# Kernel tuning notes

Hardware: AMD Instinct MI355X
Metric: run time of the kernel (lower is better)

## Reference

```python
import jax, jax.numpy as jnp
import numpy as np

K = 16          # top-k edges kept per node (init kwarg k)
TEMP = 1.0      # gumbel-softmax temperature
NEG = -1e9


def setup_inputs() -> dict:
    key = jax.random.key(0)
    ks = jax.random.split(key, 12)
    N, E, D, ED, H1, H2, OUT = 4096, 131072, 8, 8, 16, 16, 112
    x = jax.random.normal(ks[0], (N, D), jnp.float32)
    edge_index = jax.random.randint(ks[1], (2, E), 0, N, dtype=jnp.int64)
    edge_attr = jax.random.normal(ks[2], (E, ED), jnp.float32)
    node_mask = jnp.ones((N,), jnp.int32)
    # learned params
    mlp_w = jax.random.normal(ks[3], (1, ED + 2 * D), jnp.float32) * 0.1
    mlp_b = jnp.zeros((1,), jnp.float32)
    w1 = jax.random.normal(ks[4], (D, H1), jnp.float32) * (1.0 / np.sqrt(D))
    b1 = jnp.zeros((H1,), jnp.float32)
    w2 = jax.random.normal(ks[5], (H1, H2), jnp.float32) * (1.0 / np.sqrt(H1))
    b2 = jnp.zeros((H2,), jnp.float32)
    fc_w = jax.random.normal(ks[6], (H2, OUT), jnp.float32) * (1.0 / np.sqrt(H2))
    fc_b = jnp.zeros((OUT,), jnp.float32)
    return {"num_nodes": N, "edge_index": edge_index, "edge_attr": edge_attr,
            "x": x, "node_mask": node_mask, "mlp_w": mlp_w, "mlp_b": mlp_b,
            "w1": w1, "b1": b1, "w2": w2, "b2": b2, "fc_w": fc_w, "fc_b": fc_b}


def reference(num_nodes, edge_index, edge_attr, x, node_mask,
              mlp_w, mlp_b, w1, b1, w2, b2, fc_w, fc_b):
    N = num_nodes
    D = x.shape[1]
    row, col = edge_index[0], edge_index[1]

    # dense adjacency indicator (original: sparse_coo -> to_dense; used only via adj != 0)
    adj = jnp.zeros((N, N), x.dtype).at[row, col].set(1.0)

    # Linear MLP over concat([node_emb, neighbor_emb, edge_emb]) decomposes:
    # score[u,v] = x_u.w_node + adj[u,v]*(x_v.w_nbr) + (e_uv.w_edge) + b
    w_node = mlp_w[0, :D]
    w_nbr = mlp_w[0, D:2 * D]
    w_edge = mlp_w[0, 2 * D:]
    edge_s = jnp.zeros((N, N), x.dtype).at[row, col].set(edge_attr @ w_edge)
    score = (x @ w_node)[:, None] + adj * (x @ w_nbr)[None, :] + edge_s + mlp_b[0]

    score = jnp.where(adj > 0, score, NEG)
    z = jax.nn.softmax(score, axis=-1)
    z = jnp.where(adj > 0, z, NEG)
    # eval mode: gumbel noise = 0
    z = jax.nn.softmax(z / TEMP, axis=-1)

    vals, idx = jax.lax.top_k(z, K)          # (N, K)
    kth = vals[:, -1]
    topk_mask = jnp.zeros((N, N), bool).at[jnp.arange(N)[:, None], idx].set(True)

    # per-edge keep mask -> expressed as edge weight 0/1 (static shapes)
    keep = (node_mask[row] != 0) & (kth[row] != 0) & topk_mask[row, col]
    w_e = keep.astype(x.dtype)

    def gcn_conv(h, W, b):
        hW = h @ W
        deg = jnp.zeros((N,), h.dtype).at[col].add(w_e) + 1.0   # +1 self loop
        dinv = jax.lax.rsqrt(deg)
        coef = w_e * dinv[row] * dinv[col]
        agg = jnp.zeros((N, hW.shape[1]), h.dtype).at[col].add(coef[:, None] * hW[row])
        return agg + (dinv * dinv)[:, None] * hW + b            # self-loop term + bias

    # GCN (eval mode => dropout is identity)
    h = jax.nn.relu(gcn_conv(x, w1, b1))
    h = gcn_conv(h, w2, b2)
    h = jax.nn.relu(h)
    out = h @ fc_w + fc_b
    # node_mask is all ones, so x[node_mask != 0] == x
    return out
```

## Files before the change

### kernel.cpp

```cpp
#include <hip/hip_runtime.h>
#include <stdint.h>

#define N_NODES 4096
#define N_EDGES 131072
#define D_IN    8
#define NH      16
#define N_OUT   112
#define TOPK    16
#define CAP_ROW 128
#define CAP_COL 64

__global__ __launch_bounds__(256) void k_pre(
        const int* __restrict__ ei, const float* __restrict__ ea,
        const float* __restrict__ x, const float* __restrict__ mlp_w,
        const float* __restrict__ w1,
        float* __restrict__ s_nbr, float* __restrict__ h1W,
        int* __restrict__ deg_row, unsigned* __restrict__ csr,
        float* __restrict__ csr_ew) {
    int b = blockIdx.x;
    if (b < N_EDGES / 256) {
        int e = b * 256 + threadIdx.x;
        float s = 0.f;
#pragma unroll
        for (int d = 0; d < D_IN; ++d) s += ea[e * D_IN + d] * mlp_w[2 * D_IN + d];
        int r = ei[e];
        int c = ei[N_EDGES + e];
        int slot = atomicAdd(&deg_row[r], 1);
        if (slot < CAP_ROW) {
            csr[r * CAP_ROW + slot] = ((unsigned)e << 12) | (unsigned)c;
            csr_ew[r * CAP_ROW + slot] = s;
        }
    } else {
        int i = (b - N_EDGES / 256) * 256 + threadIdx.x;
        if (i >= N_NODES) return;
        float xv[D_IN];
#pragma unroll
        for (int d = 0; d < D_IN; ++d) xv[d] = x[i * D_IN + d];
        float s = 0.f;
#pragma unroll
        for (int d = 0; d < D_IN; ++d) s += xv[d] * mlp_w[D_IN + d];
        s_nbr[i] = s;
#pragma unroll
        for (int j = 0; j < NH; ++j) {
            float a = 0.f;
#pragma unroll
            for (int d = 0; d < D_IN; ++d) a += xv[d] * w1[d * NH + j];
            h1W[i * NH + j] = a;
        }
    }
}

__global__ __launch_bounds__(64) void k_topk(
        const unsigned* __restrict__ csr, const float* __restrict__ csr_ew,
        const int* __restrict__ deg_row, const float* __restrict__ s_nbr,
        const int* __restrict__ node_mask,
        int* __restrict__ deg_in, int* __restrict__ csc) {
    __shared__ unsigned s_pk[CAP_ROW];
    __shared__ float s_v[CAP_ROW];
    __shared__ unsigned char s_rep[CAP_ROW];
    __shared__ unsigned char s_kept[CAP_ROW];
    __shared__ int s_distinct;
    int r = blockIdx.x;
    int t = threadIdx.x;
    int n = deg_row[r];
    if (n > CAP_ROW) n = CAP_ROW;
    if (n == 0) return;
    for (int k = t; k < n; k += 64) {
        unsigned pk = csr[r * CAP_ROW + k];
        s_pk[k] = pk;
        s_v[k] = s_nbr[pk & 4095u] + csr_ew[r * CAP_ROW + k];
    }
    __syncthreads();
    for (int k = t; k < n; k += 64) {
        unsigned pk = s_pk[k], c = pk & 4095u;
        unsigned char rep = 1;
        for (int j = 0; j < n; ++j) {
            unsigned pj = s_pk[j];
            if ((pj & 4095u) == c && pj > pk) { rep = 0; break; }
        }
        s_rep[k] = rep;
    }
    __syncthreads();
    if (t == 0) {
        int c = 0;
        for (int j = 0; j < n; ++j) c += s_rep[j];
        s_distinct = c;
    }
    __syncthreads();
    if (s_distinct < TOPK || node_mask[r] == 0) return;
    for (int k = t; k < n; k += 64) {
        unsigned char kept = 0;
        if (s_rep[k]) {
            float vk = s_v[k];
            unsigned ck = s_pk[k] & 4095u;
            int beats = 0;
            for (int j = 0; j < n; ++j) {
                if (!s_rep[j]) continue;
                float vj = s_v[j];
                unsigned cj = s_pk[j] & 4095u;
                if (vj > vk || (vj == vk && cj < ck)) ++beats;
            }
            kept = (beats < TOPK);
        }
        s_kept[k] = kept;
    }
    __syncthreads();
    for (int k = t; k < n; k += 64) {
        unsigned c = s_pk[k] & 4095u;
        unsigned char kp = 0;
        for (int j = 0; j < n; ++j) {
            if ((s_pk[j] & 4095u) == c && s_rep[j]) { kp = s_kept[j]; break; }
        }
        if (kp) {
            int p = atomicAdd(&deg_in[(int)c], 1);
            if (p < CAP_COL) csc[(int)c * CAP_COL + p] = r;
        }
    }
}

__global__ __launch_bounds__(256) void k_gather1(
        const int* __restrict__ csc, const int* __restrict__ deg_in,
        const float* __restrict__ h1W, const float* __restrict__ b1,
        const float* __restrict__ w2, float* __restrict__ h2W) {
    int idx = blockIdx.x * 256 + threadIdx.x;
    int c = idx >> 4, f = idx & 15;
    int m = deg_in[c];
    int mm = m > CAP_COL ? CAP_COL : m;
    float acc = 0.f;
    for (int j = 0; j < mm; ++j) {
        int r = csc[c * CAP_COL + j];
        acc += rsqrtf(1.0f + (float)deg_in[r]) * h1W[r * NH + f];
    }
    float dc = rsqrtf(1.0f + (float)m);
    float v = dc * acc + dc * dc * h1W[c * NH + f] + b1[f];
    float h = v > 0.f ? v : 0.f;
    int lane = threadIdx.x & 63;
    int base = lane & 48;
    float a = 0.f;
#pragma unroll
    for (int ff = 0; ff < NH; ++ff) {
        float hv = __shfl(h, base | ff, 64);
        a += hv * w2[ff * NH + f];
    }
    h2W[c * NH + f] = a;
}

__global__ __launch_bounds__(128) void k_out(
        const int* __restrict__ csc, const int* __restrict__ deg_in,
        const float* __restrict__ h2W, const float* __restrict__ b2,
        const float* __restrict__ fc_w, const float* __restrict__ fc_b,
        float* __restrict__ out) {
    __shared__ float sh[NH];
    int c = blockIdx.x;
    int t = threadIdx.x;
    if (t < NH) {
        int m = deg_in[c];
        int mm = m > CAP_COL ? CAP_COL : m;
        float acc = 0.f;
        for (int j = 0; j < mm; ++j) {
            int r = csc[c * CAP_COL + j];
            acc += rsqrtf(1.0f + (float)deg_in[r]) * h2W[r * NH + t];
        }
        float dc = rsqrtf(1.0f + (float)m);
        float v = dc * acc + dc * dc * h2W[c * NH + t] + b2[t];
        sh[t] = v > 0.f ? v : 0.f;
    }
    __syncthreads();
    if (t < N_OUT) {
        float a = fc_b[t];
#pragma unroll
        for (int ff = 0; ff < NH; ++ff) a += sh[ff] * fc_w[ff * N_OUT + t];
        out[c * N_OUT + t] = a;
    }
}

extern "C" void kernel_launch(void* const* d_in, const int* in_sizes, int n_in,
                              void* d_out, int out_size, void* d_ws, size_t ws_size,
                              hipStream_t stream) {
    const int*   ei        = (const int*)d_in[1];
    const float* ea        = (const float*)d_in[2];
    const float* x         = (const float*)d_in[3];
    const int*   node_mask = (const int*)d_in[4];
    const float* mlp_w     = (const float*)d_in[5];
    const float* w1        = (const float*)d_in[7];
    const float* b1        = (const float*)d_in[8];
    const float* w2        = (const float*)d_in[9];
    const float* b2        = (const float*)d_in[10];
    const float* fcw       = (const float*)d_in[11];
    const float* fcb       = (const float*)d_in[12];
    float* out = (float*)d_out;

    char* ws = (char*)d_ws;
    size_t off = 0;
    auto alloc = [&](size_t bytes) -> void* {
        void* p = ws + off;
        off += (bytes + 511) & ~(size_t)511;
        return p;
    };
    int*      deg_row = (int*)alloc(N_NODES * 4);
    int*      deg_in  = (int*)alloc(N_NODES * 4);
    size_t zero_bytes = off;
    float*    s_nbr  = (float*)alloc(N_NODES * 4);
    float*    h1W    = (float*)alloc(N_NODES * NH * 4);
    float*    h2W    = (float*)alloc(N_NODES * NH * 4);
    unsigned* csr    = (unsigned*)alloc(N_NODES * CAP_ROW * 4);
    float*    csr_ew = (float*)alloc(N_NODES * CAP_ROW * 4);
    int*      csc    = (int*)alloc(N_NODES * CAP_COL * 4);
    (void)ws_size; (void)in_sizes; (void)n_in; (void)out_size;

    hipMemsetAsync(d_ws, 0, zero_bytes, stream);

    k_pre<<<N_EDGES / 256 + N_NODES / 256, 256, 0, stream>>>(
        ei, ea, x, mlp_w, w1, s_nbr, h1W, deg_row, csr, csr_ew);
    k_topk<<<N_NODES, 64, 0, stream>>>(
        csr, csr_ew, deg_row, s_nbr, node_mask, deg_in, csc);
    k_gather1<<<(N_NODES * NH) / 256, 256, 0, stream>>>(
        csc, deg_in, h1W, b1, w2, h2W);
    k_out<<<N_NODES, 128, 0, stream>>>(
        csc, deg_in, h2W, b2, fcw, fcb, out);
}
```

Measured before the change: 143.9 us.

## Fuse all stages into one cooperative persistent kernel with grid syncs

Replaces the memset and four separate kernel launches with a single cooperative kernel of 512 blocks of 256 threads. Grid-wide syncs separate zeroing, edge/CSR build, top-k selection, the first GCN layer and the output layer. This removes launch and memset overhead. In exchange it adds grid barrier costs and less parallelism per phase, since top-k now runs 4 rows per block per iteration with block-wide syncs. The output stage is also remapped to 16 threads per node.

New measurement: 383.5 us. +166.5%, slower.

```diff
diff --git a/kernel.cpp b/kernel.cpp
--- a/kernel.cpp
+++ b/kernel.cpp
@@ -1,5 +1,8 @@
 #include <hip/hip_runtime.h>
+#include <hip/hip_cooperative_groups.h>
 #include <stdint.h>
+
+namespace cg = cooperative_groups;
 
 #define N_NODES 4096
 #define N_EDGES 131072
@@ -10,16 +13,28 @@
 #define CAP_ROW 128
 #define CAP_COL 64
 
-__global__ __launch_bounds__(256) void k_pre(
+#define NBLK 512
+#define NTHR 256
+
+__global__ __launch_bounds__(256) void k_fused(
         const int* __restrict__ ei, const float* __restrict__ ea,
-        const float* __restrict__ x, const float* __restrict__ mlp_w,
-        const float* __restrict__ w1,
+        const float* __restrict__ x, const int* __restrict__ node_mask,
+        const float* __restrict__ mlp_w, const float* __restrict__ w1,
+        const float* __restrict__ b1, const float* __restrict__ w2,
+        const float* __restrict__ b2, const float* __restrict__ fc_w,
+        const float* __restrict__ fc_b, float* __restrict__ out,
+        int* __restrict__ deg_row, int* __restrict__ deg_in,
         float* __restrict__ s_nbr, float* __restrict__ h1W,
-        int* __restrict__ deg_row, unsigned* __restrict__ csr,
-        float* __restrict__ csr_ew) {
-    int b = blockIdx.x;
-    if (b < N_EDGES / 256) {
-        int e = b * 256 + threadIdx.x;
+        float* __restrict__ h2W, unsigned* __restrict__ csr,
+        float* __restrict__ csr_ew, int* __restrict__ csc) {
+    cg::grid_group grid = cg::this_grid();
+    const int tid = blockIdx.x * NTHR + threadIdx.x;
+
+    if (tid < N_NODES) { deg_row[tid] = 0; deg_in[tid] = 0; }
+    grid.sync();
+
+    {
+        const int e = tid;
         float s = 0.f;
 #pragma unroll
         for (int d = 0; d < D_IN; ++d) s += ea[e * D_IN + d] * mlp_w[2 * D_IN + d];
@@ -30,147 +45,147 @@
             csr[r * CAP_ROW + slot] = ((unsigned)e << 12) | (unsigned)c;
             csr_ew[r * CAP_ROW + slot] = s;
         }
-    } else {
-        int i = (b - N_EDGES / 256) * 256 + threadIdx.x;
-        if (i >= N_NODES) return;
+    }
+    if (tid < N_NODES) {
         float xv[D_IN];
 #pragma unroll
-        for (int d = 0; d < D_IN; ++d) xv[d] = x[i * D_IN + d];
+        for (int d = 0; d < D_IN; ++d) xv[d] = x[tid * D_IN + d];
         float s = 0.f;
 #pragma unroll
         for (int d = 0; d < D_IN; ++d) s += xv[d] * mlp_w[D_IN + d];
-        s_nbr[i] = s;
+        s_nbr[tid] = s;
 #pragma unroll
         for (int j = 0; j < NH; ++j) {
             float a = 0.f;
 #pragma unroll
             for (int d = 0; d < D_IN; ++d) a += xv[d] * w1[d * NH + j];
-            h1W[i * NH + j] = a;
-        }
-    }
-}
-
-__global__ __launch_bounds__(64) void k_topk(
-        const unsigned* __restrict__ csr, const float* __restrict__ csr_ew,
-        const int* __restrict__ deg_row, const float* __restrict__ s_nbr,
-        const int* __restrict__ node_mask,
-        int* __restrict__ deg_in, int* __restrict__ csc) {
-    __shared__ unsigned s_pk[CAP_ROW];
-    __shared__ float s_v[CAP_ROW];
-    __shared__ unsigned char s_rep[CAP_ROW];
-    __shared__ unsigned char s_kept[CAP_ROW];
-    __shared__ int s_distinct;
-    int r = blockIdx.x;
-    int t = threadIdx.x;
-    int n = deg_row[r];
-    if (n > CAP_ROW) n = CAP_ROW;
-    if (n == 0) return;
-    for (int k = t; k < n; k += 64) {
-        unsigned pk = csr[r * CAP_ROW + k];
-        s_pk[k] = pk;
-        s_v[k] = s_nbr[pk & 4095u] + csr_ew[r * CAP_ROW + k];
-    }
-    __syncthreads();
-    for (int k = t; k < n; k += 64) {
-        unsigned pk = s_pk[k], c = pk & 4095u;
-        unsigned char rep = 1;
-        for (int j = 0; j < n; ++j) {
-            unsigned pj = s_pk[j];
-            if ((pj & 4095u) == c && pj > pk) { rep = 0; break; }
-        }
-        s_rep[k] = rep;
-    }
-    __syncthreads();
-    if (t == 0) {
-        int c = 0;
-        for (int j = 0; j < n; ++j) c += s_rep[j];
-        s_distinct = c;
-    }
-    __syncthreads();
-    if (s_distinct < TOPK || node_mask[r] == 0) return;
-    for (int k = t; k < n; k += 64) {
-        unsigned char kept = 0;
-        if (s_rep[k]) {
-            float vk = s_v[k];
-            unsigned ck = s_pk[k] & 4095u;
-            int beats = 0;
-            for (int j = 0; j < n; ++j) {
-                if (!s_rep[j]) continue;
-                float vj = s_v[j];
-                unsigned cj = s_pk[j] & 4095u;
-                if (vj > vk || (vj == vk && cj < ck)) ++beats;
-            }
-            kept = (beats < TOPK);
-        }
-        s_kept[k] = kept;
-    }
-    __syncthreads();
-    for (int k = t; k < n; k += 64) {
-        unsigned c = s_pk[k] & 4095u;
-        unsigned char kp = 0;
-        for (int j = 0; j < n; ++j) {
-            if ((s_pk[j] & 4095u) == c && s_rep[j]) { kp = s_kept[j]; break; }
-        }
-        if (kp) {
-            int p = atomicAdd(&deg_in[(int)c], 1);
-            if (p < CAP_COL) csc[(int)c * CAP_COL + p] = r;
-        }
-    }
-}
-
-__global__ __launch_bounds__(256) void k_gather1(
-        const int* __restrict__ csc, const int* __restrict__ deg_in,
-        const float* __restrict__ h1W, const float* __restrict__ b1,
-        const float* __restrict__ w2, float* __restrict__ h2W) {
-    int idx = blockIdx.x * 256 + threadIdx.x;
-    int c = idx >> 4, f = idx & 15;
-    int m = deg_in[c];
-    int mm = m > CAP_COL ? CAP_COL : m;
-    float acc = 0.f;
-    for (int j = 0; j < mm; ++j) {
-        int r = csc[c * CAP_COL + j];
-        acc += rsqrtf(1.0f + (float)deg_in[r]) * h1W[r * NH + f];
-    }
-    float dc = rsqrtf(1.0f + (float)m);
-    float v = dc * acc + dc * dc * h1W[c * NH + f] + b1[f];
-    float h = v > 0.f ? v : 0.f;
-    int lane = threadIdx.x & 63;
-    int base = lane & 48;
-    float a = 0.f;
-#pragma unroll
-    for (int ff = 0; ff < NH; ++ff) {
-        float hv = __shfl(h, base | ff, 64);
-        a += hv * w2[ff * NH + f];
-    }
-    h2W[c * NH + f] = a;
-}
-
-__global__ __launch_bounds__(128) void k_out(
-        const int* __restrict__ csc, const int* __restrict__ deg_in,
-        const float* __restrict__ h2W, const float* __restrict__ b2,
-        const float* __restrict__ fc_w, const float* __restrict__ fc_b,
-        float* __restrict__ out) {
-    __shared__ float sh[NH];
-    int c = blockIdx.x;
-    int t = threadIdx.x;
-    if (t < NH) {
-        int m = deg_in[c];
-        int mm = m > CAP_COL ? CAP_COL : m;
+            h1W[tid * NH + j] = a;
+        }
+    }
+    grid.sync();
+
+    {
+        __shared__ unsigned s_pk[4][CAP_ROW];
+        __shared__ float s_v[4][CAP_ROW];
+        __shared__ unsigned char s_rep[4][CAP_ROW];
+        __shared__ unsigned char s_kept[4][CAP_ROW];
+        const int w = threadIdx.x >> 6;
+        const int t = threadIdx.x & 63;
+#pragma unroll
+        for (int it = 0; it < 2; ++it) {
+            const int r = it * 2048 + blockIdx.x * 4 + w;
+            int n = deg_row[r];
+            if (n > CAP_ROW) n = CAP_ROW;
+            for (int k = t; k < n; k += 64) {
+                unsigned pk = csr[r * CAP_ROW + k];
+                s_pk[w][k] = pk;
+                s_v[w][k] = s_nbr[pk & 4095u] + csr_ew[r * CAP_ROW + k];
+            }
+            __syncthreads();
+            for (int k = t; k < n; k += 64) {
+                unsigned pk = s_pk[w][k], c = pk & 4095u;
+                unsigned char rep = 1;
+                for (int j = 0; j < n; ++j) {
+                    unsigned pj = s_pk[w][j];
+                    if ((pj & 4095u) == c && pj > pk) { rep = 0; break; }
+                }
+                s_rep[w][k] = rep;
+            }
+            __syncthreads();
+            int cnt = 0;
+            for (int k = t; k < n; k += 64) cnt += s_rep[w][k];
+#pragma unroll
+            for (int off = 32; off; off >>= 1) cnt += __shfl_down(cnt, off, 64);
+            const int distinct = __shfl(cnt, 0, 64);
+            const bool active = (n > 0) && (distinct >= TOPK) && (node_mask[r] != 0);
+            if (active) {
+                for (int k = t; k < n; k += 64) {
+                    unsigned char kept = 0;
+                    if (s_rep[w][k]) {
+                        float vk = s_v[w][k];
+                        unsigned ck = s_pk[w][k] & 4095u;
+                        int beats = 0;
+                        for (int j = 0; j < n; ++j) {
+                            if (!s_rep[w][j]) continue;
+                            float vj = s_v[w][j];
+                            unsigned cj = s_pk[w][j] & 4095u;
+                            if (vj > vk || (vj == vk && cj < ck)) ++beats;
+                        }
+                        kept = (beats < TOPK);
+                    }
+                    s_kept[w][k] = kept;
+                }
+            }
+            __syncthreads();
+            if (active) {
+                for (int k = t; k < n; k += 64) {
+                    unsigned c = s_pk[w][k] & 4095u;
+                    unsigned char kp = 0;
+                    for (int j = 0; j < n; ++j) {
+                        if ((s_pk[w][j] & 4095u) == c && s_rep[w][j]) { kp = s_kept[w][j]; break; }
+                    }
+                    if (kp) {
+                        int p = atomicAdd(&deg_in[(int)c], 1);
+                        if (p < CAP_COL) csc[(int)c * CAP_COL + p] = r;
+                    }
+                }
+            }
+            __syncthreads();
+        }
+    }
+    grid.sync();
+
+    if (tid < N_NODES * NH) {
+        const int c = tid >> 4, f = tid & 15;
+        const int m = deg_in[c];
+        const int mm = m > CAP_COL ? CAP_COL : m;
         float acc = 0.f;
         for (int j = 0; j < mm; ++j) {
             int r = csc[c * CAP_COL + j];
-            acc += rsqrtf(1.0f + (float)deg_in[r]) * h2W[r * NH + t];
-        }
-        float dc = rsqrtf(1.0f + (float)m);
-        float v = dc * acc + dc * dc * h2W[c * NH + t] + b2[t];
-        sh[t] = v > 0.f ? v : 0.f;
-    }
-    __syncthreads();
-    if (t < N_OUT) {
-        float a = fc_b[t];
-#pragma unroll
-        for (int ff = 0; ff < NH; ++ff) a += sh[ff] * fc_w[ff * N_OUT + t];
-        out[c * N_OUT + t] = a;
+            acc += rsqrtf(1.0f + (float)deg_in[r]) * h1W[r * NH + f];
+        }
+        const float dc = rsqrtf(1.0f + (float)m);
+        float v = dc * acc + dc * dc * h1W[c * NH + f] + b1[f];
+        float h = v > 0.f ? v : 0.f;
+        const int base = (threadIdx.x & 63) & 48;
+        float a = 0.f;
+#pragma unroll
+        for (int ff = 0; ff < NH; ++ff) {
+            float hv = __shfl(h, base | ff, 64);
+            a += hv * w2[ff * NH + f];
+        }
+        h2W[c * NH + f] = a;
+    }
+    grid.sync();
+
+    {
+        const int g = tid >> 4;
+        const int f = tid & 15;
+        if (g < N_NODES) {
+            const int c = g;
+            const int m = deg_in[c];
+            const int mm = m > CAP_COL ? CAP_COL : m;
+            float acc = 0.f;
+            for (int j = 0; j < mm; ++j) {
+                int r = csc[c * CAP_COL + j];
+                acc += rsqrtf(1.0f + (float)deg_in[r]) * h2W[r * NH + f];
+            }
+            const float dc = rsqrtf(1.0f + (float)m);
+            float v = dc * acc + dc * dc * h2W[c * NH + f] + b2[f];
+            float h = v > 0.f ? v : 0.f;
+            const int base = (threadIdx.x & 63) & 48;
+#pragma unroll
+            for (int j = 0; j < 7; ++j) {
+                const int o = f + 16 * j;
+                float a = fc_b[o];
+#pragma unroll
+                for (int ff = 0; ff < NH; ++ff) {
+                    float hv = __shfl(h, base | ff, 64);
+                    a += hv * fc_w[ff * N_OUT + o];
+                }
+                out[c * N_OUT + o] = a;
+            }
+        }
     }
 }
 
@@ -199,23 +214,21 @@
     };
     int*      deg_row = (int*)alloc(N_NODES * 4);
     int*      deg_in  = (int*)alloc(N_NODES * 4);
-    size_t zero_bytes = off;
-    float*    s_nbr  = (float*)alloc(N_NODES * 4);
-    float*    h1W    = (float*)alloc(N_NODES * NH * 4);
-    float*    h2W    = (float*)alloc(N_NODES * NH * 4);
-    unsigned* csr    = (unsigned*)alloc(N_NODES * CAP_ROW * 4);
-    float*    csr_ew = (float*)alloc(N_NODES * CAP_ROW * 4);
-    int*      csc    = (int*)alloc(N_NODES * CAP_COL * 4);
+    float*    s_nbr   = (float*)alloc(N_NODES * 4);
+    float*    h1W     = (float*)alloc(N_NODES * NH * 4);
+    float*    h2W     = (float*)alloc(N_NODES * NH * 4);
+    unsigned* csr     = (unsigned*)alloc(N_NODES * CAP_ROW * 4);
+    float*    csr_ew  = (float*)alloc(N_NODES * CAP_ROW * 4);
+    int*      csc     = (int*)alloc(N_NODES * CAP_COL * 4);
     (void)ws_size; (void)in_sizes; (void)n_in; (void)out_size;
 
-    hipMemsetAsync(d_ws, 0, zero_bytes, stream);
-
-    k_pre<<<N_EDGES / 256 + N_NODES / 256, 256, 0, stream>>>(
-        ei, ea, x, mlp_w, w1, s_nbr, h1W, deg_row, csr, csr_ew);
-    k_topk<<<N_NODES, 64, 0, stream>>>(
-        csr, csr_ew, deg_row, s_nbr, node_mask, deg_in, csc);
-    k_gather1<<<(N_NODES * NH) / 256, 256, 0, stream>>>(
-        csc, deg_in, h1W, b1, w2, h2W);
-    k_out<<<N_NODES, 128, 0, stream>>>(
-        csc, deg_in, h2W, b2, fcw, fcb, out);
+    void* args[] = {
+        (void*)&ei, (void*)&ea, (void*)&x, (void*)&node_mask, (void*)&mlp_w,
+        (void*)&w1, (void*)&b1, (void*)&w2, (void*)&b2, (void*)&fcw,
+        (void*)&fcb, (void*)&out, (void*)&deg_row, (void*)&deg_in,
+        (void*)&s_nbr, (void*)&h1W, (void*)&h2W, (void*)&csr,
+        (void*)&csr_ew, (void*)&csc
+    };
+    hipLaunchCooperativeKernel((void*)k_fused, dim3(NBLK), dim3(NTHR),
+                               args, 0, stream);
 }
```

## Split neighbor gathers across wavefront lanes and vectorize edge/node loads

Applied to the files above, without the earlier changes.

Both GCN aggregation kernels now assign one 64-lane wavefront per node, with four lane groups each summing a strided share of the incoming edges and combining via xor shuffles. The output kernel drops its shared-memory stage and block-wide barrier, computing the 112 outputs from wavefront shuffles. The pre-pass loads edge attributes and node features as float4 pairs. This aims to cut serial per-thread gather latency and launch overhead in the small gather kernels, but the dominant top-k kernel is unchanged, so the total effect is bounded.

Measured after the change: 132.1 us. 8.2% less time.

```diff
diff --git a/kernel.cpp b/kernel.cpp
--- a/kernel.cpp
+++ b/kernel.cpp
@@ -20,9 +20,11 @@
     int b = blockIdx.x;
     if (b < N_EDGES / 256) {
         int e = b * 256 + threadIdx.x;
-        float s = 0.f;
-#pragma unroll
-        for (int d = 0; d < D_IN; ++d) s += ea[e * D_IN + d] * mlp_w[2 * D_IN + d];
+        const float4* ea4 = (const float4*)ea;
+        float4 a0 = ea4[2 * e], a1 = ea4[2 * e + 1];
+        float s = a0.x * mlp_w[16] + a0.y * mlp_w[17] + a0.z * mlp_w[18] +
+                  a0.w * mlp_w[19] + a1.x * mlp_w[20] + a1.y * mlp_w[21] +
+                  a1.z * mlp_w[22] + a1.w * mlp_w[23];
         int r = ei[e];
         int c = ei[N_EDGES + e];
         int slot = atomicAdd(&deg_row[r], 1);
@@ -33,9 +35,9 @@
     } else {
         int i = (b - N_EDGES / 256) * 256 + threadIdx.x;
         if (i >= N_NODES) return;
-        float xv[D_IN];
-#pragma unroll
-        for (int d = 0; d < D_IN; ++d) xv[d] = x[i * D_IN + d];
+        const float4* x4 = (const float4*)x;
+        float4 v0 = x4[2 * i], v1 = x4[2 * i + 1];
+        float xv[D_IN] = {v0.x, v0.y, v0.z, v0.w, v1.x, v1.y, v1.z, v1.w};
         float s = 0.f;
 #pragma unroll
         for (int d = 0; d < D_IN; ++d) s += xv[d] * mlp_w[D_IN + d];
@@ -122,56 +124,62 @@
         const int* __restrict__ csc, const int* __restrict__ deg_in,
         const float* __restrict__ h1W, const float* __restrict__ b1,
         const float* __restrict__ w2, float* __restrict__ h2W) {
-    int idx = blockIdx.x * 256 + threadIdx.x;
-    int c = idx >> 4, f = idx & 15;
-    int m = deg_in[c];
-    int mm = m > CAP_COL ? CAP_COL : m;
+    const int lane = threadIdx.x & 63;
+    const int c = blockIdx.x * 4 + (threadIdx.x >> 6);
+    const int f = lane & 15;
+    const int jj = lane >> 4;
+    const int m = deg_in[c];
+    const int mm = m > CAP_COL ? CAP_COL : m;
     float acc = 0.f;
-    for (int j = 0; j < mm; ++j) {
+    for (int j = jj; j < mm; j += 4) {
         int r = csc[c * CAP_COL + j];
         acc += rsqrtf(1.0f + (float)deg_in[r]) * h1W[r * NH + f];
     }
-    float dc = rsqrtf(1.0f + (float)m);
+    acc += __shfl_xor(acc, 16, 64);
+    acc += __shfl_xor(acc, 32, 64);
+    const float dc = rsqrtf(1.0f + (float)m);
     float v = dc * acc + dc * dc * h1W[c * NH + f] + b1[f];
     float h = v > 0.f ? v : 0.f;
-    int lane = threadIdx.x & 63;
-    int base = lane & 48;
     float a = 0.f;
 #pragma unroll
     for (int ff = 0; ff < NH; ++ff) {
-        float hv = __shfl(h, base | ff, 64);
+        float hv = __shfl(h, ff, 64);
         a += hv * w2[ff * NH + f];
     }
-    h2W[c * NH + f] = a;
-}
-
-__global__ __launch_bounds__(128) void k_out(
+    if (jj == 0) h2W[c * NH + f] = a;
+}
+
+__global__ __launch_bounds__(256) void k_out(
         const int* __restrict__ csc, const int* __restrict__ deg_in,
         const float* __restrict__ h2W, const float* __restrict__ b2,
         const float* __restrict__ fc_w, const float* __restrict__ fc_b,
         float* __restrict__ out) {
-    __shared__ float sh[NH];
-    int c = blockIdx.x;
-    int t = threadIdx.x;
-    if (t < NH) {
-        int m = deg_in[c];
-        int mm = m > CAP_COL ? CAP_COL : m;
-        float acc = 0.f;
-        for (int j = 0; j < mm; ++j) {
-            int r = csc[c * CAP_COL + j];
-            acc += rsqrtf(1.0f + (float)deg_in[r]) * h2W[r * NH + t];
-        }
-        float dc = rsqrtf(1.0f + (float)m);
-        float v = dc * acc + dc * dc * h2W[c * NH + t] + b2[t];
-        sh[t] = v > 0.f ? v : 0.f;
-    }
-    __syncthreads();
-    if (t < N_OUT) {
-        float a = fc_b[t];
-#pragma unroll
-        for (int ff = 0; ff < NH; ++ff) a += sh[ff] * fc_w[ff * N_OUT + t];
-        out[c * N_OUT + t] = a;
-    }
+    const int lane = threadIdx.x & 63;
+    const int c = blockIdx.x * 4 + (threadIdx.x >> 6);
+    const int f = lane & 15;
+    const int jj = lane >> 4;
+    const int m = deg_in[c];
+    const int mm = m > CAP_COL ? CAP_COL : m;
+    float acc = 0.f;
+    for (int j = jj; j < mm; j += 4) {
+        int r = csc[c * CAP_COL + j];
+        acc += rsqrtf(1.0f + (float)deg_in[r]) * h2W[r * NH + f];
+    }
+    acc += __shfl_xor(acc, 16, 64);
+    acc += __shfl_xor(acc, 32, 64);
+    const float dc = rsqrtf(1.0f + (float)m);
+    float v = dc * acc + dc * dc * h2W[c * NH + f] + b2[f];
+    float h = v > 0.f ? v : 0.f;
+    float a0 = fc_b[lane];
+    float a1 = (lane < N_OUT - 64) ? fc_b[64 + lane] : 0.f;
+#pragma unroll
+    for (int ff = 0; ff < NH; ++ff) {
+        float hv = __shfl(h, ff, 64);
+        a0 += hv * fc_w[ff * N_OUT + lane];
+        if (lane < N_OUT - 64) a1 += hv * fc_w[ff * N_OUT + 64 + lane];
+    }
+    out[c * N_OUT + lane] = a0;
+    if (lane < N_OUT - 64) out[c * N_OUT + 64 + lane] = a1;
 }
 
 extern "C" void kernel_launch(void* const* d_in, const int* in_sizes, int n_in,
@@ -214,8 +222,8 @@
         ei, ea, x, mlp_w, w1, s_nbr, h1W, deg_row, csr, csr_ew);
     k_topk<<<N_NODES, 64, 0, stream>>>(
         csr, csr_ew, deg_row, s_nbr, node_mask, deg_in, csc);
-    k_gather1<<<(N_NODES * NH) / 256, 256, 0, stream>>>(
+    k_gather1<<<N_NODES / 4, 256, 0, stream>>>(
         csc, deg_in, h1W, b1, w2, h2W);
-    k_out<<<N_NODES, 128, 0, stream>>>(
+    k_out<<<N_NODES / 4, 256, 0, stream>>>(
         csc, deg_in, h2W, b2, fcw, fcb, out);
 }
```
